# Performance work log

Measured on AMD Instinct MI355X. Metric: run time of the kernel, lower is better.

The kernel has to match this reference:

```python
import jax, jax.numpy as jnp
import numpy as np

B, C_ENT, C_REL = 32768, 1000, 500


def setup_inputs() -> dict:
    key = jax.random.key(0)
    ks = jax.random.split(key, 6)
    return {
        "sub_input": jax.random.normal(ks[0], (B, C_ENT), dtype=jnp.float32),
        "relation_input": jax.random.normal(ks[1], (B, C_REL), dtype=jnp.float32),
        "obj_input": jax.random.normal(ks[2], (B, C_ENT), dtype=jnp.float32),
        "sub_target": jax.random.randint(ks[3], (B,), 0, C_ENT, dtype=jnp.int32),
        "relation_target": jax.random.randint(ks[4], (B,), 0, C_REL, dtype=jnp.int32),
        "obj_target": jax.random.randint(ks[5], (B,), 0, C_ENT, dtype=jnp.int32),
    }


def reference(sub_input, relation_input, obj_input, sub_target, relation_target, obj_target):
    s = jax.nn.softmax(sub_input, axis=1)
    r = jax.nn.softmax(relation_input, axis=1)
    o = jax.nn.softmax(obj_input, axis=1)
    b = s.shape[0]
    rows = jnp.arange(b)

    # ground-truth triplet probability
    gt = s[rows, sub_target] * r[rows, relation_target] * o[rows, obj_target]

    # top-2 values/indices per row (replaces full torch.sort)
    sv, si = jax.lax.top_k(s, 2)
    rv, ri = jax.lax.top_k(r, 2)
    ov, oi = jax.lax.top_k(o, 2)

    # all three argmaxes match the targets?
    cond = (si[:, 0] == sub_target) & (ri[:, 0] == relation_target) & (oi[:, 0] == obj_target)

    # 8 combinations of top-2 probs; second-smallest of the 8 (torch.sort ascending, index 1)
    tmp = (sv[:, :, None, None] * rv[:, None, :, None] * ov[:, None, None, :]).reshape(b, 8)
    second_smallest = jnp.sort(tmp, axis=1)[:, 1]

    top1 = sv[:, 0] * rv[:, 0] * ov[:, 0]
    pre = jnp.where(cond, second_smallest, top1)

    out = 1.0 - gt + pre
    return jnp.mean(jnp.maximum(out, 0.0))
```

## Files before the change

kernel.cpp:

```cpp
#include <hip/hip_runtime.h>
#include <float.h>
#include <limits.h>


constexpr int B      = 32768;
constexpr int C_ENT  = 1000;
constexpr int C_REL  = 500;


template<int NK, int C4>
__device__ inline float4 wave_stats(const float* __restrict__ row, int lane, int target) {
  const float4* row4 = (const float4*)row;
  float4 v[NK];
#pragma unroll
  for (int k = 0; k < NK; ++k) {
    int i = lane + 64 * k;
    v[k] = (i < C4) ? row4[i] : make_float4(-FLT_MAX, -FLT_MAX, -FLT_MAX, -FLT_MAX);
  }
  float xt = row[target];

  float lm = -FLT_MAX;
#pragma unroll
  for (int k = 0; k < NK; ++k)
    lm = fmaxf(lm, fmaxf(fmaxf(v[k].x, v[k].y), fmaxf(v[k].z, v[k].w)));
#pragma unroll
  for (int off = 32; off; off >>= 1)
    lm = fmaxf(lm, __shfl_xor(lm, off));
  const float m1 = lm;

  float z[NK];
  float m2 = -FLT_MAX;
  int   idx = INT_MAX;
  int   cnt = 0;
#pragma unroll
  for (int k = 0; k < NK; ++k) {
    const int base = 4 * (lane + 64 * k);
    const float a0 = v[k].x, a1 = v[k].y, a2 = v[k].z, a3 = v[k].w;
    z[k] = (__expf(a0 - m1) + __expf(a1 - m1)) + (__expf(a2 - m1) + __expf(a3 - m1));
    const bool e0 = (a0 == m1), e1 = (a1 == m1), e2 = (a2 == m1), e3 = (a3 == m1);
    cnt += (int)e0 + (int)e1 + (int)e2 + (int)e3;
    m2 = fmaxf(m2, fmaxf(e0 ? -FLT_MAX : a0, e1 ? -FLT_MAX : a1));
    m2 = fmaxf(m2, fmaxf(e2 ? -FLT_MAX : a2, e3 ? -FLT_MAX : a3));
    const int i01 = min(e0 ? base     : INT_MAX, e1 ? base + 1 : INT_MAX);
    const int i23 = min(e2 ? base + 2 : INT_MAX, e3 ? base + 3 : INT_MAX);
    idx = min(idx, min(i01, i23));
  }
  float Z;
  if constexpr (NK == 4) Z = (z[0] + z[1]) + (z[2] + z[3]);
  else                   Z = z[0] + z[1];

#pragma unroll
  for (int off = 32; off; off >>= 1) {
    Z   += __shfl_xor(Z, off);
    m2   = fmaxf(m2, __shfl_xor(m2, off));
    cnt += __shfl_xor(cnt, off);
    idx  = min(idx, __shfl_xor(idx, off));
  }
  if (cnt >= 2) m2 = m1;

  const float invZ = 1.0f / Z;
  return make_float4(invZ,
                     __expf(m2 - m1) * invZ,
                     __expf(xt - m1) * invZ,
                     __int_as_float(idx));
}

__global__ __launch_bounds__(256) void stats_kernel(
    const float* __restrict__ s, const float* __restrict__ r, const float* __restrict__ o,
    const int* __restrict__ st, const int* __restrict__ rt, const int* __restrict__ ot,
    float4* __restrict__ out4) {
  const int wid  = threadIdx.x >> 6;
  const int lane = threadIdx.x & 63;
  const int gw   = blockIdx.x * 4 + wid;
  const int m    = gw >> 15;
  const int row  = gw & (B - 1);
  float4 res;
  if (m == 0)      res = wave_stats<4, C_ENT / 4>(s + (size_t)row * C_ENT, lane, st[row]);
  else if (m == 1) res = wave_stats<4, C_ENT / 4>(o + (size_t)row * C_ENT, lane, ot[row]);
  else             res = wave_stats<2, C_REL / 4>(r + (size_t)row * C_REL, lane, rt[row]);
  if (lane == 0) out4[m * B + row] = res;
}

__global__ __launch_bounds__(256) void combine_kernel(
    const float4* __restrict__ stat4,
    const int* __restrict__ st, const int* __restrict__ rt, const int* __restrict__ ot,
    float* __restrict__ partial) {
  const int row = blockIdx.x * 256 + threadIdx.x;
  const float4 S = stat4[row];
  const float4 O = stat4[B + row];
  const float4 R = stat4[2 * B + row];
  const float gt   = S.z * R.z * O.z;
  const float top1 = S.x * R.x * O.x;
  const float c1 = S.x * R.y * O.y;
  const float c2 = S.y * R.x * O.y;
  const float c3 = S.y * R.y * O.x;
  const float second = fminf(c1, fminf(c2, c3));
  const bool cond = (__float_as_int(S.w) == st[row]) &&
                    (__float_as_int(R.w) == rt[row]) &&
                    (__float_as_int(O.w) == ot[row]);
  const float pre = cond ? second : top1;
  partial[row] = fmaxf(1.0f - gt + pre, 0.0f);
}


__device__ inline void combine_stats(float& m1, int& i1, float& m2, float& Z,
                                     float bm1, int bi1, float bm2, float bZ) {
  bool bwin = (bm1 > m1) || (bm1 == m1 && bi1 < i1);
  float wm1 = bwin ? bm1 : m1;
  int   wi1 = bwin ? bi1 : i1;
  float wm2 = bwin ? bm2 : m2;
  float lm1 = bwin ? m1  : bm1;
  float wZ  = bwin ? bZ  : Z;
  float lZ  = bwin ? Z   : bZ;
  m1 = wm1; i1 = wi1;
  m2 = fmaxf(wm2, lm1);
  Z  = wZ + lZ * __expf(lm1 - wm1);
}

template<int NK, int C4>
__device__ inline void row_stats(const float* __restrict__ row, int lane, int target,
                                 float& p_top1, float& p_top2, int& amax, float& p_tgt) {
  const float4* row4 = (const float4*)row;
  float4 v[NK];
#pragma unroll
  for (int k = 0; k < NK; ++k) {
    int idx = lane + 64 * k;
    v[k] = (idx < C4) ? row4[idx] : make_float4(-FLT_MAX, -FLT_MAX, -FLT_MAX, -FLT_MAX);
  }
  float m1 = -FLT_MAX, m2 = -FLT_MAX;
  int   i1 = 0x7fffffff;
#pragma unroll
  for (int k = 0; k < NK; ++k) {
    int base = 4 * (lane + 64 * k);
    float a0 = v[k].x, a1 = v[k].y, a2 = v[k].z, a3 = v[k].w;
    if (a0 > m1) { m2 = m1; m1 = a0; i1 = base;     } else if (a0 > m2) m2 = a0;
    if (a1 > m1) { m2 = m1; m1 = a1; i1 = base + 1; } else if (a1 > m2) m2 = a1;
    if (a2 > m1) { m2 = m1; m1 = a2; i1 = base + 2; } else if (a2 > m2) m2 = a2;
    if (a3 > m1) { m2 = m1; m1 = a3; i1 = base + 3; } else if (a3 > m2) m2 = a3;
  }
  float Z = 0.f;
#pragma unroll
  for (int k = 0; k < NK; ++k) {
    Z += __expf(v[k].x - m1); Z += __expf(v[k].y - m1);
    Z += __expf(v[k].z - m1); Z += __expf(v[k].w - m1);
  }
#pragma unroll
  for (int off = 32; off > 0; off >>= 1) {
    float bm1 = __shfl_xor(m1, off);
    int   bi1 = __shfl_xor(i1, off);
    float bm2 = __shfl_xor(m2, off);
    float bZ  = __shfl_xor(Z,  off);
    combine_stats(m1, i1, m2, Z, bm1, bi1, bm2, bZ);
  }
  float invZ = 1.0f / Z;
  float xt   = row[target];
  p_top1 = invZ;
  p_top2 = __expf(m2 - m1) * invZ;
  p_tgt  = __expf(xt - m1) * invZ;
  amax   = i1;
}

template<bool ATOMIC>
__global__ __launch_bounds__(256) void rank_loss_kernel(
    const float* __restrict__ s, const float* __restrict__ r, const float* __restrict__ o,
    const int* __restrict__ st, const int* __restrict__ rt, const int* __restrict__ ot,
    float* __restrict__ partial, float* __restrict__ out) {
  const int wid  = threadIdx.x >> 6;
  const int lane = threadIdx.x & 63;
  const int row  = blockIdx.x * 4 + wid;

  const float* srow = s + (size_t)row * C_ENT;
  const float* rrow = r + (size_t)row * C_REL;
  const float* orow = o + (size_t)row * C_ENT;
  const int tS = st[row], tR = rt[row], tO = ot[row];

  float sp0, sp1, spt; int sa;
  float rp0, rp1, rpt; int ra;
  float op0, op1, opt; int oa;
  row_stats<4, C_ENT / 4>(srow, lane, tS, sp0, sp1, sa, spt);
  row_stats<2, C_REL / 4>(rrow, lane, tR, rp0, rp1, ra, rpt);
  row_stats<4, C_ENT / 4>(orow, lane, tO, op0, op1, oa, opt);

  if (lane == 0) {
    float gt   = spt * rpt * opt;
    float top1 = sp0 * rp0 * op0;
    float c1 = sp0 * rp1 * op1;
    float c2 = sp1 * rp0 * op1;
    float c3 = sp1 * rp1 * op0;
    float second = fminf(c1, fminf(c2, c3));
    bool cond = (sa == tS) && (ra == tR) && (oa == tO);
    float pre = cond ? second : top1;
    float val = fmaxf(1.0f - gt + pre, 0.0f);
    if (ATOMIC) atomicAdd(out, val * (1.0f / (float)B));
    else        partial[row] = val;
  }
}


__global__ __launch_bounds__(1024) void reduce_sum_kernel(const float* __restrict__ p,
                                                          float* __restrict__ out) {
  const float4* p4 = (const float4*)p;
  float sum = 0.f;
  for (int i = threadIdx.x; i < B / 4; i += 1024) {
    float4 v = p4[i];
    sum += (v.x + v.y) + (v.z + v.w);
  }
#pragma unroll
  for (int off = 32; off > 0; off >>= 1) sum += __shfl_xor(sum, off);
  __shared__ float lds[16];
  if ((threadIdx.x & 63) == 0) lds[threadIdx.x >> 6] = sum;
  __syncthreads();
  if (threadIdx.x == 0) {
    float t = 0.f;
#pragma unroll
    for (int i = 0; i < 16; ++i) t += lds[i];
    out[0] = t * (1.0f / (float)B);
  }
}

extern "C" void kernel_launch(void* const* d_in, const int* in_sizes, int n_in,
                              void* d_out, int out_size, void* d_ws, size_t ws_size,
                              hipStream_t stream) {
  const float* s  = (const float*)d_in[0];
  const float* r  = (const float*)d_in[1];
  const float* o  = (const float*)d_in[2];
  const int*   st = (const int*)d_in[3];
  const int*   rt = (const int*)d_in[4];
  const int*   ot = (const int*)d_in[5];
  float* out = (float*)d_out;

  const size_t statBytes = (size_t)3 * B * sizeof(float4);
  if (ws_size >= statBytes + (size_t)B * sizeof(float)) {
    float4* stat4  = (float4*)d_ws;
    float* partial = (float*)((char*)d_ws + statBytes);
    stats_kernel<<<3 * B / 4, 256, 0, stream>>>(s, r, o, st, rt, ot, stat4);
    combine_kernel<<<B / 256, 256, 0, stream>>>(stat4, st, rt, ot, partial);
    reduce_sum_kernel<<<1, 1024, 0, stream>>>(partial, out);
  } else if (ws_size >= (size_t)B * sizeof(float)) {
    float* partial = (float*)d_ws;
    rank_loss_kernel<false><<<B / 4, 256, 0, stream>>>(s, r, o, st, rt, ot, partial, nullptr);
    reduce_sum_kernel<<<1, 1024, 0, stream>>>(partial, out);
  } else {
    hipMemsetAsync(d_out, 0, sizeof(float), stream);
    rank_loss_kernel<true><<<B / 4, 256, 0, stream>>>(s, r, o, st, rt, ot, nullptr, out);
  }
}
```

Baseline: 319.4 us.

## Software-pipeline row loads across persistent waves and use exp2 intrinsic

The stats kernel now gives each wave several rows (4 entity rows or 8 relation rows) and prefetches the next row's data into registers while it computes softmax stats for the current one. The grid shrinks from one wave per row to 5120 blocks, and the launch bound raises the occupancy hint. Exponentials are rewritten as exp2 with a folded log2e FMA through the AMDGCN builtin. The intent is to hide memory latency in a bandwidth-bound pass, at the cost of higher register pressure and fewer waves in flight.

```diff
diff --git a/kernel.cpp b/kernel.cpp
--- a/kernel.cpp
+++ b/kernel.cpp
@@ -3,40 +3,54 @@
 #include <limits.h>
 
 
-constexpr int B      = 32768;
-constexpr int C_ENT  = 1000;
-constexpr int C_REL  = 500;
-
+constexpr int B     = 32768;
+constexpr int C_ENT = 1000;
+constexpr int C_REL = 500;
+constexpr float LOG2E = 1.4426950408889634f;
+
+__device__ inline float fast_exp2(float x) {
+#if __has_builtin(__builtin_amdgcn_exp2f)
+  return __builtin_amdgcn_exp2f(x);
+#else
+  return exp2f(x);
+#endif
+}
+
+template<int NK>
+struct UnitData { float4 v[NK]; float xt; };
 
 template<int NK, int C4>
-__device__ inline float4 wave_stats(const float* __restrict__ row, int lane, int target) {
+__device__ inline void unit_load(const float* __restrict__ row, int lane, int target,
+                                 UnitData<NK>& U) {
   const float4* row4 = (const float4*)row;
-  float4 v[NK];
-#pragma unroll
-  for (int k = 0; k < NK; ++k) {
-    int i = lane + 64 * k;
-    v[k] = (i < C4) ? row4[i] : make_float4(-FLT_MAX, -FLT_MAX, -FLT_MAX, -FLT_MAX);
-  }
-  float xt = row[target];
-
+#pragma unroll
+  for (int k = 0; k < NK; ++k) {
+    U.v[k] = make_float4(-FLT_MAX, -FLT_MAX, -FLT_MAX, -FLT_MAX);
+    const int i = lane + 64 * k;
+    if (i < C4) U.v[k] = row4[i];
+  }
+  U.xt = row[target];
+}
+
+template<int NK>
+__device__ inline float4 unit_compute(const UnitData<NK>& U, int lane) {
   float lm = -FLT_MAX;
 #pragma unroll
   for (int k = 0; k < NK; ++k)
-    lm = fmaxf(lm, fmaxf(fmaxf(v[k].x, v[k].y), fmaxf(v[k].z, v[k].w)));
-#pragma unroll
-  for (int off = 32; off; off >>= 1)
-    lm = fmaxf(lm, __shfl_xor(lm, off));
+    lm = fmaxf(lm, fmaxf(fmaxf(U.v[k].x, U.v[k].y), fmaxf(U.v[k].z, U.v[k].w)));
+#pragma unroll
+  for (int off = 32; off; off >>= 1) lm = fmaxf(lm, __shfl_xor(lm, off));
   const float m1 = lm;
-
-  float z[NK];
-  float m2 = -FLT_MAX;
-  int   idx = INT_MAX;
-  int   cnt = 0;
+  const float nm1l = -m1 * LOG2E;
+
+  float Z = 0.f, m2 = -FLT_MAX;
+  int idx = INT_MAX, cnt = 0;
 #pragma unroll
   for (int k = 0; k < NK; ++k) {
     const int base = 4 * (lane + 64 * k);
-    const float a0 = v[k].x, a1 = v[k].y, a2 = v[k].z, a3 = v[k].w;
-    z[k] = (__expf(a0 - m1) + __expf(a1 - m1)) + (__expf(a2 - m1) + __expf(a3 - m1));
+    const float a0 = U.v[k].x, a1 = U.v[k].y, a2 = U.v[k].z, a3 = U.v[k].w;
+    Z += (fast_exp2(fmaf(a0, LOG2E, nm1l)) + fast_exp2(fmaf(a1, LOG2E, nm1l))) +
+         (fast_exp2(fmaf(a2, LOG2E, nm1l)) + fast_exp2(fmaf(a3, LOG2E, nm1l)));
     const bool e0 = (a0 == m1), e1 = (a1 == m1), e2 = (a2 == m1), e3 = (a3 == m1);
     cnt += (int)e0 + (int)e1 + (int)e2 + (int)e3;
     m2 = fmaxf(m2, fmaxf(e0 ? -FLT_MAX : a0, e1 ? -FLT_MAX : a1));
@@ -45,10 +59,6 @@
     const int i23 = min(e2 ? base + 2 : INT_MAX, e3 ? base + 3 : INT_MAX);
     idx = min(idx, min(i01, i23));
   }
-  float Z;
-  if constexpr (NK == 4) Z = (z[0] + z[1]) + (z[2] + z[3]);
-  else                   Z = z[0] + z[1];
-
 #pragma unroll
   for (int off = 32; off; off >>= 1) {
     Z   += __shfl_xor(Z, off);
@@ -60,25 +70,55 @@
 
   const float invZ = 1.0f / Z;
   return make_float4(invZ,
-                     __expf(m2 - m1) * invZ,
-                     __expf(xt - m1) * invZ,
+                     fast_exp2((m2 - m1) * LOG2E) * invZ,
+                     fast_exp2(fmaf(U.xt, LOG2E, nm1l)) * invZ,
                      __int_as_float(idx));
 }
 
-__global__ __launch_bounds__(256) void stats_kernel(
+template<int NK, int C4, int NSTEP>
+__device__ inline void pipe_run(const float* (&rp)[NSTEP], int (&tg)[NSTEP],
+                                int (&oi)[NSTEP], int lane, float4* __restrict__ out4) {
+  UnitData<NK> A, B;
+  unit_load<NK, C4>(rp[0], lane, tg[0], A);
+#pragma unroll
+  for (int step = 0; step < NSTEP; ++step) {
+    if (step + 1 < NSTEP) unit_load<NK, C4>(rp[step + 1], lane, tg[step + 1], B);
+    const float4 res = unit_compute<NK>(A, lane);
+    if (lane == 0) out4[oi[step]] = res;
+    A = B;
+  }
+}
+
+__global__ __launch_bounds__(256, 8) void stats_pipe_kernel(
     const float* __restrict__ s, const float* __restrict__ r, const float* __restrict__ o,
     const int* __restrict__ st, const int* __restrict__ rt, const int* __restrict__ ot,
     float4* __restrict__ out4) {
-  const int wid  = threadIdx.x >> 6;
   const int lane = threadIdx.x & 63;
-  const int gw   = blockIdx.x * 4 + wid;
-  const int m    = gw >> 15;
-  const int row  = gw & (B - 1);
-  float4 res;
-  if (m == 0)      res = wave_stats<4, C_ENT / 4>(s + (size_t)row * C_ENT, lane, st[row]);
-  else if (m == 1) res = wave_stats<4, C_ENT / 4>(o + (size_t)row * C_ENT, lane, ot[row]);
-  else             res = wave_stats<2, C_REL / 4>(r + (size_t)row * C_REL, lane, rt[row]);
-  if (lane == 0) out4[m * B + row] = res;
+  const int gw   = blockIdx.x * 4 + (threadIdx.x >> 6);
+  if (gw < 16384) {
+    const float* rp[4]; int tg[4]; int oi[4];
+#pragma unroll
+    for (int t = 0; t < 4; ++t) {
+      const int u   = gw + 16384 * t;
+      const int m   = u >> 15;
+      const int row = u & (B - 1);
+      rp[t] = (m ? o : s) + (size_t)row * C_ENT;
+      tg[t] = (m ? ot : st)[row];
+      oi[t] = m * B + row;
+    }
+    pipe_run<4, C_ENT / 4, 4>(rp, tg, oi, lane, out4);
+  } else {
+    const int w2 = gw - 16384;
+    const float* rp[8]; int tg[8]; int oi[8];
+#pragma unroll
+    for (int t = 0; t < 8; ++t) {
+      const int row = w2 + 4096 * t;
+      rp[t] = r + (size_t)row * C_REL;
+      tg[t] = rt[row];
+      oi[t] = 2 * B + row;
+    }
+    pipe_run<2, C_REL / 4, 8>(rp, tg, oi, lane, out4);
+  }
 }
 
 __global__ __launch_bounds__(256) void combine_kernel(
@@ -102,6 +142,27 @@
   partial[row] = fmaxf(1.0f - gt + pre, 0.0f);
 }
 
+__global__ __launch_bounds__(1024) void reduce_sum_kernel(const float* __restrict__ p,
+                                                          float* __restrict__ out) {
+  const float4* p4 = (const float4*)p;
+  float sum = 0.f;
+  for (int i = threadIdx.x; i < B / 4; i += 1024) {
+    const float4 v = p4[i];
+    sum += (v.x + v.y) + (v.z + v.w);
+  }
+#pragma unroll
+  for (int off = 32; off > 0; off >>= 1) sum += __shfl_xor(sum, off);
+  __shared__ float lds[16];
+  if ((threadIdx.x & 63) == 0) lds[threadIdx.x >> 6] = sum;
+  __syncthreads();
+  if (threadIdx.x == 0) {
+    float t = 0.f;
+#pragma unroll
+    for (int i = 0; i < 16; ++i) t += lds[i];
+    out[0] = t * (1.0f / (float)B);
+  }
+}
+
 
 __device__ inline void combine_stats(float& m1, int& i1, float& m2, float& Z,
                                      float bm1, int bi1, float bm2, float bZ) {
@@ -160,26 +221,21 @@
   amax   = i1;
 }
 
-template<bool ATOMIC>
-__global__ __launch_bounds__(256) void rank_loss_kernel(
+__global__ __launch_bounds__(256) void rank_loss_atomic_kernel(
     const float* __restrict__ s, const float* __restrict__ r, const float* __restrict__ o,
     const int* __restrict__ st, const int* __restrict__ rt, const int* __restrict__ ot,
-    float* __restrict__ partial, float* __restrict__ out) {
+    float* __restrict__ out) {
   const int wid  = threadIdx.x >> 6;
   const int lane = threadIdx.x & 63;
   const int row  = blockIdx.x * 4 + wid;
 
-  const float* srow = s + (size_t)row * C_ENT;
-  const float* rrow = r + (size_t)row * C_REL;
-  const float* orow = o + (size_t)row * C_ENT;
   const int tS = st[row], tR = rt[row], tO = ot[row];
-
   float sp0, sp1, spt; int sa;
   float rp0, rp1, rpt; int ra;
   float op0, op1, opt; int oa;
-  row_stats<4, C_ENT / 4>(srow, lane, tS, sp0, sp1, sa, spt);
-  row_stats<2, C_REL / 4>(rrow, lane, tR, rp0, rp1, ra, rpt);
-  row_stats<4, C_ENT / 4>(orow, lane, tO, op0, op1, oa, opt);
+  row_stats<4, C_ENT / 4>(s + (size_t)row * C_ENT, lane, tS, sp0, sp1, sa, spt);
+  row_stats<2, C_REL / 4>(r + (size_t)row * C_REL, lane, tR, rp0, rp1, ra, rpt);
+  row_stats<4, C_ENT / 4>(o + (size_t)row * C_ENT, lane, tO, op0, op1, oa, opt);
 
   if (lane == 0) {
     float gt   = spt * rpt * opt;
@@ -190,31 +246,7 @@
     float second = fminf(c1, fminf(c2, c3));
     bool cond = (sa == tS) && (ra == tR) && (oa == tO);
     float pre = cond ? second : top1;
-    float val = fmaxf(1.0f - gt + pre, 0.0f);
-    if (ATOMIC) atomicAdd(out, val * (1.0f / (float)B));
-    else        partial[row] = val;
-  }
-}
-
-
-__global__ __launch_bounds__(1024) void reduce_sum_kernel(const float* __restrict__ p,
-                                                          float* __restrict__ out) {
-  const float4* p4 = (const float4*)p;
-  float sum = 0.f;
-  for (int i = threadIdx.x; i < B / 4; i += 1024) {
-    float4 v = p4[i];
-    sum += (v.x + v.y) + (v.z + v.w);
-  }
-#pragma unroll
-  for (int off = 32; off > 0; off >>= 1) sum += __shfl_xor(sum, off);
-  __shared__ float lds[16];
-  if ((threadIdx.x & 63) == 0) lds[threadIdx.x >> 6] = sum;
-  __syncthreads();
-  if (threadIdx.x == 0) {
-    float t = 0.f;
-#pragma unroll
-    for (int i = 0; i < 16; ++i) t += lds[i];
-    out[0] = t * (1.0f / (float)B);
+    atomicAdd(out, fmaxf(1.0f - gt + pre, 0.0f) * (1.0f / (float)B));
   }
 }
 
@@ -233,15 +265,11 @@
   if (ws_size >= statBytes + (size_t)B * sizeof(float)) {
     float4* stat4  = (float4*)d_ws;
     float* partial = (float*)((char*)d_ws + statBytes);
-    stats_kernel<<<3 * B / 4, 256, 0, stream>>>(s, r, o, st, rt, ot, stat4);
+    stats_pipe_kernel<<<5120, 256, 0, stream>>>(s, r, o, st, rt, ot, stat4);
     combine_kernel<<<B / 256, 256, 0, stream>>>(stat4, st, rt, ot, partial);
-    reduce_sum_kernel<<<1, 1024, 0, stream>>>(partial, out);
-  } else if (ws_size >= (size_t)B * sizeof(float)) {
-    float* partial = (float*)d_ws;
-    rank_loss_kernel<false><<<B / 4, 256, 0, stream>>>(s, r, o, st, rt, ot, partial, nullptr);
     reduce_sum_kernel<<<1, 1024, 0, stream>>>(partial, out);
   } else {
     hipMemsetAsync(d_out, 0, sizeof(float), stream);
-    rank_loss_kernel<true><<<B / 4, 256, 0, stream>>>(s, r, o, st, rt, ot, nullptr, out);
-  }
-}
+    rank_loss_atomic_kernel<<<B / 4, 256, 0, stream>>>(s, r, o, st, rt, ot, out);
+  }
+}
```

After: 334.7 us. +4.8%, slower.
